# Optimization experiments

Measured on AMD Instinct MI355X. Metric: run time of the kernel, lower is better.

## Reference

```python
import jax, jax.numpy as jnp
import numpy as np

ATTN_SCALE = 0.12
HEAD_DIM = 128


def _rms_norm(x):
    # F.rms_norm with no weight; eps defaults to machine eps of dtype
    eps = jnp.asarray(jnp.finfo(x.dtype).eps, x.dtype)
    return x * jax.lax.rsqrt(jnp.mean(x * x, axis=-1, keepdims=True) + eps)


def _rope(x):
    # x: [B, T, H, D]; standard rotary over (first-half, second-half) pairs
    T, D = x.shape[1], x.shape[-1]
    half = D // 2
    inv_freq = 1.0 / (10000.0 ** (jnp.arange(half, dtype=jnp.float32) / half))
    ang = jnp.arange(T, dtype=jnp.float32)[:, None] * inv_freq[None, :]  # [T, half]
    cos = jnp.cos(ang)[None, :, None, :].astype(x.dtype)
    sin = jnp.sin(ang)[None, :, None, :].astype(x.dtype)
    x1, x2 = x[..., :half], x[..., half:]
    return jnp.concatenate([x1 * cos - x2 * sin, x1 * sin + x2 * cos], axis=-1)


def setup_inputs() -> dict:
    key = jax.random.key(0)
    ks = jax.random.split(key, 4)
    B, T, dim, H, hd = 4, 2048, 1024, 8, HEAD_DIM
    hdim = H * hd
    std = 0.5 * dim ** (-0.5)
    bound = (3.0 ** 0.5) * std
    return {
        "x": jax.random.normal(ks[0], (B, T, dim), jnp.float32),
        "ve": jax.random.normal(ks[1], (B, T, hdim), jnp.float32),
        "qkv_w": jax.random.uniform(ks[2], (3, hdim, dim), jnp.float32, -bound, bound),
        "lambdas": jnp.array([0.5, 0.5], jnp.float32),
        "c_proj_w": jax.random.normal(ks[3], (dim, hdim), jnp.float32) * (hdim ** -0.5),
        "c_proj_b": jnp.zeros((dim,), jnp.float32),
    }


def reference(x, ve, qkv_w, lambdas, c_proj_w, c_proj_b):
    B, T, dim = x.shape
    hdim = qkv_w.shape[1]
    hd = HEAD_DIM
    H = hdim // hd
    # fused QKV projection: [B,T,3,H,hd]
    qkv = jnp.einsum('btd,ehd->bteh', x, qkv_w.reshape(3 * hdim, dim).reshape(3 * H, hd, dim).reshape(3 * hdim // hd, hd, dim))
    qkv = jnp.einsum('btd,fd->btf', x, qkv_w.reshape(3 * hdim, dim)).reshape(B, T, 3, H, hd)
    q, k, v = qkv[:, :, 0], qkv[:, :, 1], qkv[:, :, 2]  # each [B,T,H,hd]
    q, k = _rms_norm(q), _rms_norm(k)
    q, k = _rope(q), _rope(k)
    v = lambdas[0] * v + lambdas[1] * ve.reshape(B, T, H, hd)
    # causal SDPA with custom scale
    scores = jnp.einsum('bthd,bshd->bhts', q, k) * ATTN_SCALE  # [B,H,T,T]
    causal = jnp.tril(jnp.ones((T, T), dtype=bool))
    scores = jnp.where(causal[None, None], scores, jnp.finfo(scores.dtype).min)
    p = jax.nn.softmax(scores, axis=-1)
    y = jnp.einsum('bhts,bshd->bthd', p, v).reshape(B, T, hdim)
    return y @ c_proj_w.T + c_proj_b
```

## Files before the change

kernel.cpp:

```cpp
#include <hip/hip_runtime.h>
#include <math.h>

typedef unsigned short u16;
typedef short bf16x8 __attribute__((ext_vector_type(8)));
typedef u16 u16x2 __attribute__((ext_vector_type(2)));
typedef u16 u16x4 __attribute__((ext_vector_type(4)));
typedef u16 u16x8 __attribute__((ext_vector_type(8)));
typedef float f32x2 __attribute__((ext_vector_type(2)));
typedef float f32x4 __attribute__((ext_vector_type(4)));
typedef float f32x16 __attribute__((ext_vector_type(16)));

typedef __attribute__((address_space(1))) const void gvoid_t;
typedef __attribute__((address_space(3))) void lvoid_t;

__device__ __forceinline__ u16 f2bf(float f) {
  union { float f; unsigned u; } v; v.f = f;
  unsigned r = v.u + 0x7fffu + ((v.u >> 16) & 1u);
  return (u16)(r >> 16);
}
__device__ __forceinline__ float bf2f(u16 h) {
  union { unsigned u; float f; } v; v.u = ((unsigned)h) << 16;
  return v.f;
}
__device__ __forceinline__ f32x4 mfma16(bf16x8 a, bf16x8 b, f32x4 c) {
  return __builtin_amdgcn_mfma_f32_16x16x32_bf16(a, b, c, 0, 0, 0);
}
__device__ __forceinline__ f32x16 mfma32(bf16x8 a, bf16x8 b, f32x16 c) {
  return __builtin_amdgcn_mfma_f32_32x32x16_bf16(a, b, c, 0, 0, 0);
}
__device__ __forceinline__ void gload_lds16(const void* g, void* l) {
  __builtin_amdgcn_global_load_lds((gvoid_t*)g, (lvoid_t*)l, 16, 0, 0);
}
__device__ __forceinline__ unsigned cvtpk_bf16(float lo, float hi) {
  unsigned r;
  asm("v_cvt_pk_bf16_f32 %0, %1, %2" : "=v"(r) : "v"(lo), "v"(hi));
  return r;
}
__device__ __forceinline__ void pswap32(unsigned& a, unsigned& b) {
  asm("v_permlane32_swap_b32 %0, %1" : "+v"(a), "+v"(b));
}

#define BAR() __builtin_amdgcn_s_barrier()
#define WAITLGKM()                          \
  asm volatile("s_waitcnt lgkmcnt(0)");     \
  __builtin_amdgcn_sched_barrier(0)
#define WAITVM(N)                                \
  asm volatile("s_waitcnt vmcnt(" #N ")");       \
  __builtin_amdgcn_sched_barrier(0)

__global__ __launch_bounds__(256) void cvt_bf16_kernel(const float* __restrict__ in,
                                                       u16* __restrict__ out, int n4) {
  int i = blockIdx.x * 256 + threadIdx.x;
  if (i >= n4) return;
  f32x4 v = *(const f32x4*)(in + (size_t)i * 4);
  u16x4 o;
  o[0] = f2bf(v[0]); o[1] = f2bf(v[1]); o[2] = f2bf(v[2]); o[3] = f2bf(v[3]);
  *(u16x4*)(out + (size_t)i * 4) = o;
}

__global__ __launch_bounds__(256) void rope_tab_kernel(float* __restrict__ ct,
                                                       float* __restrict__ st) {
  int i = blockIdx.x * 256 + threadIdx.x;
  int t = i >> 6, j = i & 63;
  float inv = powf(10000.f, -(float)j * (1.0f / 64.0f));
  float ang = (float)t * inv;
  ct[i] = cosf(ang);
  st[i] = sinf(ang);
}

template <int BM, int OUTF32>
__global__ __launch_bounds__(512, 1) void gemm8p_kernel(
    const u16* __restrict__ A, const u16* __restrict__ B, void* __restrict__ C,
    const float* __restrict__ bias, int M, int N, int K, int nbn) {
  constexpr int AH = BM / 2;
  constexpr int WR = AH / 2;
  constexpr int MI = WR / 16;
  constexpr int NACC = 2 * MI;
  constexpr int AROUNDS = AH / 64;
  __shared__ u16 Alds[2][BM * 64];
  __shared__ u16 Blds[2][256 * 64];
  int nwg = gridDim.x;
  int cpx = nwg >> 3;
  int bid = blockIdx.x;
  int swz = (bid & 7) * cpx + (bid >> 3);
  int bm = swz / nbn, bn = swz % nbn;
  size_t m0 = (size_t)bm * BM, n0 = (size_t)bn * 256;
  int tid = threadIdx.x, wid = tid >> 6, lane = tid & 63;
  int wr = wid >> 2, wc = wid & 3, l15 = lane & 15, l4 = lane >> 4;
  int srow = tid >> 3, sch = tid & 7;

  const u16* Abase = A + m0 * K;
  const u16* Bbase = B + n0 * K;

  f32x4 acc[NACC][4];
#pragma unroll
  for (int m = 0; m < NACC; m++)
#pragma unroll
    for (int n = 0; n < 4; n++) acc[m][n] = f32x4{0.f, 0.f, 0.f, 0.f};

  auto stageA = [&](int buf, int kt, int half) {
#pragma unroll
    for (int r = 0; r < AROUNDS; ++r) {
      int row = AH * half + 64 * r + srow;
      gload_lds16(Abase + (size_t)row * K + kt * 64 + 8 * (sch ^ (row & 7)),
                  &Alds[buf][(AH * half + 64 * r + 8 * wid) * 64]);
    }
  };
  auto stageB = [&](int buf, int kt, int half) {
#pragma unroll
    for (int r = 0; r < 2; ++r) {
      int row = 128 * half + 64 * r + srow;
      gload_lds16(Bbase + (size_t)row * K + kt * 64 + 8 * (sch ^ (row & 7)),
                  &Blds[buf][(128 * half + 64 * r + 8 * wid) * 64]);
    }
  };
  auto rdA = [&](int buf, int half, bf16x8 (&a)[MI][2]) {
#pragma unroll
    for (int mi = 0; mi < MI; ++mi)
#pragma unroll
      for (int kk = 0; kk < 2; ++kk) {
        int row = AH * half + WR * wr + 16 * mi + l15;
        a[mi][kk] = *(const bf16x8*)((const char*)(&Alds[buf][0]) + row * 128 +
                                     ((kk * 64 + 16 * l4) ^ ((row & 7) << 4)));
      }
  };
  auto rdB = [&](int buf, int half, bf16x8 (&bb)[2][2]) {
#pragma unroll
    for (int ni = 0; ni < 2; ++ni)
#pragma unroll
      for (int kk = 0; kk < 2; ++kk) {
        int row = 64 * wc + 32 * half + 16 * ni + l15;
        bb[ni][kk] = *(const bf16x8*)((const char*)(&Blds[buf][0]) + row * 128 +
                                      ((kk * 64 + 16 * l4) ^ ((row & 7) << 4)));
      }
  };

#define QUAD(AF, BF, MH, NH)                                              \
  do {                                                                    \
    __builtin_amdgcn_s_setprio(1);                                        \
    _Pragma("unroll") for (int mi = 0; mi < MI; ++mi)                     \
        _Pragma("unroll") for (int ni = 0; ni < 2; ++ni)                  \
            _Pragma("unroll") for (int kk = 0; kk < 2; ++kk)              \
                acc[MI * MH + mi][2 * NH + ni] =                          \
        mfma16(AF[mi][kk], BF[ni][kk], acc[MI * MH + mi][2 * NH + ni]);   \
    __builtin_amdgcn_s_setprio(0);                                        \
  } while (0)

  stageB(0, 0, 0);
  stageB(0, 0, 1);
  stageA(0, 0, 0);
  stageA(0, 0, 1);
  if constexpr (BM == 256) { WAITVM(2); } else { WAITVM(1); }
  BAR();

  int nk = K >> 6;
  bf16x8 a0[MI][2], a1[MI][2], b0[2][2], b1[2][2];
  for (int t = 0; t < nk; ++t) {
    int buf = t & 1, nxt = buf ^ 1;
    bool pf = (t + 1 < nk);
    rdA(buf, 0, a0);
    rdB(buf, 0, b0);
    if (pf) stageB(nxt, t + 1, 0);
    BAR();
    WAITLGKM();
    QUAD(a0, b0, 0, 0);
    BAR();
    rdB(buf, 1, b1);
    if (pf) stageB(nxt, t + 1, 1);
    BAR();
    WAITLGKM();
    QUAD(a0, b1, 0, 1);
    if (pf) { WAITVM(4); } else { WAITVM(0); }
    BAR();
    rdA(buf, 1, a1);
    if (pf) stageA(nxt, t + 1, 0);
    BAR();
    WAITLGKM();
    QUAD(a1, b0, 1, 0);
    BAR();
    if (pf) stageA(nxt, t + 1, 1);
    BAR();
    QUAD(a1, b1, 1, 1);
    if (pf) {
      if constexpr (BM == 256) { WAITVM(2); } else { WAITVM(1); }
    }
    BAR();
  }

#pragma unroll
  for (int mi = 0; mi < NACC; ++mi) {
#pragma unroll
    for (int ni = 0; ni < 4; ++ni) {
      size_t row = m0 + AH * (mi / MI) + WR * wr + 16 * (mi % MI) + 4 * l4;
      size_t col = n0 + 64 * wc + 16 * ni + l15;
#pragma unroll
      for (int i = 0; i < 4; ++i) {
        float v = acc[mi][ni][i];
        if constexpr (OUTF32) {
          ((float*)C)[(row + i) * N + col] = v + bias[col];
        } else {
          ((u16*)C)[(row + i) * N + col] = f2bf(v);
        }
      }
    }
  }
#undef QUAD
}

__global__ __launch_bounds__(256) void transform_kernel(
    const u16* __restrict__ qkv, const float* __restrict__ ve,
    const float* __restrict__ lam, const float* __restrict__ ct,
    const float* __restrict__ st, u16* __restrict__ qn, u16* __restrict__ kn,
    u16* __restrict__ vt) {
  constexpr int T = 2048, HD = 128;
  __shared__ u16 vtile[64][132];
  int tt = blockIdx.x, bh = blockIdx.y;
  int b = bh >> 3, h = bh & 7;
  int tid = threadIdx.x, wid = tid >> 6, lane = tid & 63;
  float l0 = lam[0], l1 = lam[1];
  int d0 = 2 * lane;
  float sgn = (lane < 32) ? -1.f : 1.f;
#pragma unroll 1
  for (int j = 0; j < 16; ++j) {
    int tl = wid * 16 + j;
    int t = tt * 64 + tl;
    size_t base = ((size_t)(b * T + t)) * 3072 + h * HD + d0;
    u16x2 qraw = *(const u16x2*)(qkv + base);
    u16x2 kraw = *(const u16x2*)(qkv + base + 1024);
    u16x2 vraw = *(const u16x2*)(qkv + base + 2048);
    f32x2 vef = *(const f32x2*)(ve + ((size_t)(b * T + t)) * 1024 + h * HD + d0);
    float q0 = bf2f(qraw[0]), q1 = bf2f(qraw[1]);
    float k0 = bf2f(kraw[0]), k1 = bf2f(kraw[1]);
    float sq = q0 * q0 + q1 * q1, sk = k0 * k0 + k1 * k1;
#pragma unroll
    for (int m = 1; m < 64; m <<= 1) {
      sq += __shfl_xor(sq, m);
      sk += __shfl_xor(sk, m);
    }
    float qs = rsqrtf(sq * (1.f / 128.f) + 1.1920929e-7f);
    float ks = rsqrtf(sk * (1.f / 128.f) + 1.1920929e-7f);
    q0 *= qs; q1 *= qs; k0 *= ks; k1 *= ks;
    int jj = d0 & 63;
    f32x2 c2 = *(const f32x2*)(ct + t * 64 + jj);
    f32x2 s2 = *(const f32x2*)(st + t * 64 + jj);
    float q0p = __shfl_xor(q0, 32), q1p = __shfl_xor(q1, 32);
    float k0p = __shfl_xor(k0, 32), k1p = __shfl_xor(k1, 32);
    u16x2 oq, ok;
    oq[0] = f2bf(q0 * c2[0] + sgn * q0p * s2[0]);
    oq[1] = f2bf(q1 * c2[1] + sgn * q1p * s2[1]);
    ok[0] = f2bf(k0 * c2[0] + sgn * k0p * s2[0]);
    ok[1] = f2bf(k1 * c2[1] + sgn * k1p * s2[1]);
    size_t orow = ((size_t)bh * T + t) * HD + d0;
    *(u16x2*)(qn + orow) = oq;
    *(u16x2*)(kn + orow) = ok;
    vtile[tl][d0] = f2bf(l0 * bf2f(vraw[0]) + l1 * vef[0]);
    vtile[tl][d0 + 1] = f2bf(l0 * bf2f(vraw[1]) + l1 * vef[1]);
  }
  __syncthreads();
#pragma unroll
  for (int it = 0; it < 4; ++it) {
    int ci = it * 256 + tid;
    int d = ci >> 3, c8 = ci & 7;
    u16x8 o;
#pragma unroll
    for (int u = 0; u < 8; u++) o[u] = vtile[c8 * 8 + u][d];
    *(u16x8*)(vt + ((size_t)bh * HD + d) * T + tt * 64 + c8 * 8) = o;
  }
}

__global__ __launch_bounds__(256, 2) void attn_kernel(
    const u16* __restrict__ Qn, const u16* __restrict__ Kn,
    const u16* __restrict__ Vt, u16* __restrict__ Y) {
  constexpr int T = 2048;
  __shared__ u16 Klds[2][64 * 128];
  __shared__ u16 Vlds[2][128 * 64];
  int bid = blockIdx.x;
  int g = bid >> 5;
  int s = (g < 8) ? (15 - g) : (g - 8);
  int bh = bid & 31;
  int b = bh >> 3, h = bh & 7;
  int tid = threadIdx.x, wid = tid >> 6, lane = tid & 63;
  int l31 = lane & 31, hh = lane >> 5;
  const u16* Qb = Qn + (size_t)bh * T * 128;
  const u16* Kb = Kn + (size_t)bh * T * 128;
  const u16* Vb = Vt + (size_t)bh * 128 * T;
  int q0w = s * 128 + wid * 32;
  int qmaxw = q0w + 31;
  int ktend = 2 * s + 2;
  int qg = q0w + l31;

  bf16x8 qf[8];
  {
    const u16* qr = Qb + (size_t)(q0w + l31) * 128 + 8 * hh;
#pragma unroll
    for (int ks = 0; ks < 8; ks++) qf[ks] = *(const bf16x8*)(qr + 16 * ks);
  }
  f32x16 acc[4];
#pragma unroll
  for (int mt = 0; mt < 4; mt++)
#pragma unroll
    for (int r = 0; r < 16; r++) acc[mt][r] = 0.f;
  float m_run = -1e30f, l_run = 0.f;

  auto stage = [&](int buf, int kt) {
#pragma unroll
    for (int it = 0; it < 4; ++it) {
      int id = wid * 256 + it * 64 + lane;
      int r = id >> 4, c = id & 15;
      gload_lds16(Kb + (size_t)(kt * 64 + r) * 128 + 8 * (c ^ (r & 7)),
                  &Klds[buf][(size_t)(wid * 256 + it * 64) * 8]);
      int rv = id >> 3, cv = id & 7;
      gload_lds16(Vb + (size_t)rv * T + kt * 64 + 8 * (cv ^ (rv & 7)),
                  &Vlds[buf][(size_t)(wid * 256 + it * 64) * 8]);
    }
  };

  stage(0, 0);
  __syncthreads();

  for (int kt = 0; kt < ktend; ++kt) {
    int cur = kt & 1;
    if (kt + 1 < ktend) stage(cur ^ 1, kt + 1);
    if (kt * 64 <= qmaxw) {
      const char* kb = (const char*)&Klds[cur][0];
      const char* vb = (const char*)&Vlds[cur][0];
      int rswz = (l31 & 7) << 4;
      f32x16 st0, st1;
#pragma unroll
      for (int r = 0; r < 16; r++) { st0[r] = 0.f; st1[r] = 0.f; }
#pragma unroll
      for (int ks = 0; ks < 8; ks++) {
        bf16x8 kf0 = *(const bf16x8*)(kb + ((l31 * 256 + 32 * ks + 16 * hh) ^ rswz));
        bf16x8 kf1 = *(const bf16x8*)(kb + (((32 + l31) * 256 + 32 * ks + 16 * hh) ^ rswz));
        st0 = mfma32(kf0, qf[ks], st0);
        st1 = mfma32(kf1, qf[ks], st1);
      }
      bool edge = (kt == (qmaxw >> 6));
      if (edge) {
#pragma unroll
        for (int r = 0; r < 16; r++) {
          int kvb = kt * 64 + (r & 3) + 8 * (r >> 2) + 4 * hh;
          if (kvb > qg) st0[r] = -1e30f;
          if (kvb + 32 > qg) st1[r] = -1e30f;
        }
      }
      float m8[8];
#pragma unroll
      for (int r = 0; r < 8; r++)
        m8[r] = fmaxf(fmaxf(st0[r], st0[r + 8]), fmaxf(st1[r], st1[r + 8]));
#pragma unroll
      for (int r = 0; r < 4; r++) m8[r] = fmaxf(m8[r], m8[r + 4]);
      float pm = fmaxf(fmaxf(m8[0], m8[1]), fmaxf(m8[2], m8[3]));
      pm = fmaxf(pm, __shfl_xor(pm, 32));
      float pmn = pm * 0.12f;
      bool nos = __all(pmn <= m_run + 8.0f);
      float mnew = nos ? m_run : fmaxf(m_run, pmn);
      if (!nos) {
        float alpha = __expf(m_run - mnew);
        l_run *= alpha;
#pragma unroll
        for (int mt = 0; mt < 4; mt++)
#pragma unroll
          for (int r = 0; r < 16; r++) acc[mt][r] *= alpha;
        m_run = mnew;
      }
      float sa = 0.f, sb = 0.f, sc = 0.f, sd = 0.f;
#pragma unroll
      for (int r = 0; r < 4; r++) {
        st0[r]      = __expf(fmaf(st0[r],      0.12f, -mnew)); sa += st0[r];
        st0[r + 4]  = __expf(fmaf(st0[r + 4],  0.12f, -mnew)); sb += st0[r + 4];
        st0[r + 8]  = __expf(fmaf(st0[r + 8],  0.12f, -mnew)); sc += st0[r + 8];
        st0[r + 12] = __expf(fmaf(st0[r + 12], 0.12f, -mnew)); sd += st0[r + 12];
        st1[r]      = __expf(fmaf(st1[r],      0.12f, -mnew)); sa += st1[r];
        st1[r + 4]  = __expf(fmaf(st1[r + 4],  0.12f, -mnew)); sb += st1[r + 4];
        st1[r + 8]  = __expf(fmaf(st1[r + 8],  0.12f, -mnew)); sc += st1[r + 8];
        st1[r + 12] = __expf(fmaf(st1[r + 12], 0.12f, -mnew)); sd += st1[r + 12];
      }
      float ps = (sa + sb) + (sc + sd);
      ps += __shfl_xor(ps, 32);
      l_run += ps;
      unsigned pA0[4], pB0[4], pA1[4], pB1[4];
#pragma unroll
      for (int rr = 0; rr < 4; rr++) {
        pA0[rr] = cvtpk_bf16(st0[4 * rr], st0[4 * rr + 1]);
        pB0[rr] = cvtpk_bf16(st0[4 * rr + 2], st0[4 * rr + 3]);
        pA1[rr] = cvtpk_bf16(st1[4 * rr], st1[4 * rr + 1]);
        pB1[rr] = cvtpk_bf16(st1[4 * rr + 2], st1[4 * rr + 3]);
      }
      bf16x8 pf[4];
#pragma unroll
      for (int ks2 = 0; ks2 < 4; ks2++) {
        int k1 = ks2 & 1;
        unsigned a0, b0, a1, b1;
        if (ks2 < 2) { a0 = pA0[2 * k1]; b0 = pA0[2 * k1 + 1]; a1 = pB0[2 * k1]; b1 = pB0[2 * k1 + 1]; }
        else         { a0 = pA1[2 * k1]; b0 = pA1[2 * k1 + 1]; a1 = pB1[2 * k1]; b1 = pB1[2 * k1 + 1]; }
        pswap32(a0, b0);
        pswap32(a1, b1);
        union { unsigned w[4]; bf16x8 v; } u;
        u.w[0] = a0; u.w[1] = a1; u.w[2] = b0; u.w[3] = b1;
        pf[ks2] = u.v;
      }
#pragma unroll
      for (int mt = 0; mt < 4; mt++) {
        int row = 32 * mt + l31;
#pragma unroll
        for (int ks2 = 0; ks2 < 4; ks2++) {
          bf16x8 vf = *(const bf16x8*)(vb + ((row * 128 + 32 * ks2 + 16 * hh) ^ rswz));
          acc[mt] = mfma32(vf, pf[ks2], acc[mt]);
        }
      }
    }
    __syncthreads();
  }
  float linv = 1.f / l_run;
  size_t yrow = (size_t)b * T + q0w + l31;
  u16* yp = Y + yrow * 1024 + h * 128;
#pragma unroll
  for (int mt = 0; mt < 4; mt++) {
#pragma unroll
    for (int rr = 0; rr < 4; rr++) {
      u16x4 o;
#pragma unroll
      for (int i = 0; i < 4; i++) o[i] = f2bf(acc[mt][4 * rr + i] * linv);
      *(u16x4*)(yp + 32 * mt + 8 * rr + 4 * hh) = o;
    }
  }
}

extern "C" void kernel_launch(void* const* d_in, const int* in_sizes, int n_in,
                              void* d_out, int out_size, void* d_ws, size_t ws_size,
                              hipStream_t stream) {
  (void)in_sizes; (void)n_in; (void)out_size; (void)ws_size;
  const float* x = (const float*)d_in[0];
  const float* ve = (const float*)d_in[1];
  const float* qkvw = (const float*)d_in[2];
  const float* lam = (const float*)d_in[3];
  const float* cpw = (const float*)d_in[4];
  const float* cpb = (const float*)d_in[5];
  float* out = (float*)d_out;
  char* ws = (char*)d_ws;

  u16* xb   = (u16*)(ws + 0);
  u16* wqkv = (u16*)(ws + 16777216);
  u16* wp   = (u16*)(ws + 23068672);
  u16* qkv  = (u16*)(ws + 25165824);
  u16* qn   = (u16*)(ws + 75497472);
  u16* kn   = (u16*)(ws + 92274688);
  u16* vt   = (u16*)(ws + 109051904);
  float* ctab = (float*)(ws + 125829120);
  float* stab = (float*)(ws + 126353408);
  u16* y = xb;

  rope_tab_kernel<<<512, 256, 0, stream>>>(ctab, stab);
  cvt_bf16_kernel<<<8192, 256, 0, stream>>>(x, xb, 2097152);
  cvt_bf16_kernel<<<3072, 256, 0, stream>>>(qkvw, wqkv, 786432);
  cvt_bf16_kernel<<<1024, 256, 0, stream>>>(cpw, wp, 262144);
  gemm8p_kernel<128, 0><<<768, 512, 0, stream>>>(xb, wqkv, qkv, nullptr, 8192, 3072, 1024, 12);
  transform_kernel<<<dim3(32, 32), 256, 0, stream>>>(qkv, ve, lam, ctab, stab, qn, kn, vt);
  attn_kernel<<<512, 256, 0, stream>>>(qn, kn, vt, y);
  gemm8p_kernel<128, 1><<<256, 512, 0, stream>>>(y, wp, out, cpb, 8192, 1024, 1024, 4);
}
```

Measured before the change: 209.8 us.

## Rework GEMM prefetch schedule, vectorize transform, use exp2 softmax and MFMA priority

The GEMM now issues the A and B prefetches for the next K-tile earlier and interleaved, with vmcnt waits computed from per-stage load counts. The QKV GEMM switches to BM=256 tiles with half the workgroups. The transform kernel is vectorized to 8 elements per lane using 16-lane row groups, with a padded LDS tile. The attention softmax uses hardware exp2 with a pre-scaled log2e factor, and the MFMA blocks are raised in wave priority. Together these target global-load latency, instruction count and scheduling, at the risk of wrong vmcnt accounting and changed occupancy or tile balance.

```diff
diff --git a/kernel.cpp b/kernel.cpp
--- a/kernel.cpp
+++ b/kernel.cpp
@@ -40,13 +40,25 @@
   asm("v_permlane32_swap_b32 %0, %1" : "+v"(a), "+v"(b));
 }
 
+#if __has_builtin(__builtin_amdgcn_exp2f)
+#define EXPW(x) __builtin_amdgcn_exp2f(x)
+#define SCALE_W 0.17312354f
+#define DEFER_THR 11.5415603f
+#else
+#define EXPW(x) __expf(x)
+#define SCALE_W 0.12f
+#define DEFER_THR 8.0f
+#endif
+
 #define BAR() __builtin_amdgcn_s_barrier()
 #define WAITLGKM()                          \
   asm volatile("s_waitcnt lgkmcnt(0)");     \
   __builtin_amdgcn_sched_barrier(0)
-#define WAITVM(N)                                \
-  asm volatile("s_waitcnt vmcnt(" #N ")");       \
-  __builtin_amdgcn_sched_barrier(0)
+#define WAITVMC(N)                                    \
+  do {                                                \
+    __builtin_amdgcn_s_waitcnt(0x0F70 | (N));         \
+    __builtin_amdgcn_sched_barrier(0);                \
+  } while (0)
 
 __global__ __launch_bounds__(256) void cvt_bf16_kernel(const float* __restrict__ in,
                                                        u16* __restrict__ out, int n4) {
@@ -77,6 +89,8 @@
   constexpr int MI = WR / 16;
   constexpr int NACC = 2 * MI;
   constexpr int AROUNDS = AH / 64;
+  constexpr int SA = AROUNDS;
+  constexpr int SB = 2;
   __shared__ u16 Alds[2][BM * 64];
   __shared__ u16 Blds[2][256 * 64];
   int nwg = gridDim.x;
@@ -147,10 +161,10 @@
   } while (0)
 
   stageB(0, 0, 0);
+  stageA(0, 0, 0);
   stageB(0, 0, 1);
-  stageA(0, 0, 0);
   stageA(0, 0, 1);
-  if constexpr (BM == 256) { WAITVM(2); } else { WAITVM(1); }
+  WAITVMC(SA + SB);
   BAR();
 
   int nk = K >> 6;
@@ -160,30 +174,27 @@
     bool pf = (t + 1 < nk);
     rdA(buf, 0, a0);
     rdB(buf, 0, b0);
-    if (pf) stageB(nxt, t + 1, 0);
+    if (pf) { stageB(nxt, t + 1, 0); stageA(nxt, t + 1, 0); }
     BAR();
     WAITLGKM();
     QUAD(a0, b0, 0, 0);
+    if (pf) { WAITVMC(2 * SA + SB); } else { WAITVMC(SA); }
     BAR();
     rdB(buf, 1, b1);
     if (pf) stageB(nxt, t + 1, 1);
     BAR();
     WAITLGKM();
     QUAD(a0, b1, 0, 1);
-    if (pf) { WAITVM(4); } else { WAITVM(0); }
+    if (pf) { WAITVMC(2 * SB + SA); } else { WAITVMC(0); }
     BAR();
     rdA(buf, 1, a1);
-    if (pf) stageA(nxt, t + 1, 0);
+    if (pf) stageA(nxt, t + 1, 1);
     BAR();
     WAITLGKM();
     QUAD(a1, b0, 1, 0);
     BAR();
-    if (pf) stageA(nxt, t + 1, 1);
-    BAR();
     QUAD(a1, b1, 1, 1);
-    if (pf) {
-      if constexpr (BM == 256) { WAITVM(2); } else { WAITVM(1); }
-    }
+    if (pf) WAITVMC(SA + SB);
     BAR();
   }
 
@@ -212,49 +223,62 @@
     const float* __restrict__ lam, const float* __restrict__ ct,
     const float* __restrict__ st, u16* __restrict__ qn, u16* __restrict__ kn,
     u16* __restrict__ vt) {
-  constexpr int T = 2048, HD = 128;
-  __shared__ u16 vtile[64][132];
+  constexpr int T = 2048;
+  __shared__ u16 vtile[64][136];
   int tt = blockIdx.x, bh = blockIdx.y;
   int b = bh >> 3, h = bh & 7;
   int tid = threadIdx.x, wid = tid >> 6, lane = tid & 63;
+  int lsub = lane & 15, lrow = lane >> 4;
   float l0 = lam[0], l1 = lam[1];
-  int d0 = 2 * lane;
-  float sgn = (lane < 32) ? -1.f : 1.f;
-#pragma unroll 1
-  for (int j = 0; j < 16; ++j) {
-    int tl = wid * 16 + j;
+  int d0 = 8 * lsub;
+  float sgn = (lsub < 8) ? -1.f : 1.f;
+  int jj = d0 & 63;
+#pragma unroll
+  for (int it = 0; it < 4; ++it) {
+    int tl = wid * 16 + it * 4 + lrow;
     int t = tt * 64 + tl;
-    size_t base = ((size_t)(b * T + t)) * 3072 + h * HD + d0;
-    u16x2 qraw = *(const u16x2*)(qkv + base);
-    u16x2 kraw = *(const u16x2*)(qkv + base + 1024);
-    u16x2 vraw = *(const u16x2*)(qkv + base + 2048);
-    f32x2 vef = *(const f32x2*)(ve + ((size_t)(b * T + t)) * 1024 + h * HD + d0);
-    float q0 = bf2f(qraw[0]), q1 = bf2f(qraw[1]);
-    float k0 = bf2f(kraw[0]), k1 = bf2f(kraw[1]);
-    float sq = q0 * q0 + q1 * q1, sk = k0 * k0 + k1 * k1;
-#pragma unroll
-    for (int m = 1; m < 64; m <<= 1) {
+    size_t base = ((size_t)(b * T + t)) * 3072 + h * 128 + d0;
+    u16x8 qraw = *(const u16x8*)(qkv + base);
+    u16x8 kraw = *(const u16x8*)(qkv + base + 1024);
+    u16x8 vraw = *(const u16x8*)(qkv + base + 2048);
+    const float* vep = ve + ((size_t)(b * T + t)) * 1024 + h * 128 + d0;
+    f32x4 ve0 = *(const f32x4*)(vep);
+    f32x4 ve1 = *(const f32x4*)(vep + 4);
+    float q[8], k[8];
+    float sq = 0.f, sk = 0.f;
+#pragma unroll
+    for (int i = 0; i < 8; ++i) {
+      q[i] = bf2f(qraw[i]); k[i] = bf2f(kraw[i]);
+      sq += q[i] * q[i]; sk += k[i] * k[i];
+    }
+#pragma unroll
+    for (int m = 1; m < 16; m <<= 1) {
       sq += __shfl_xor(sq, m);
       sk += __shfl_xor(sk, m);
     }
     float qs = rsqrtf(sq * (1.f / 128.f) + 1.1920929e-7f);
     float ks = rsqrtf(sk * (1.f / 128.f) + 1.1920929e-7f);
-    q0 *= qs; q1 *= qs; k0 *= ks; k1 *= ks;
-    int jj = d0 & 63;
-    f32x2 c2 = *(const f32x2*)(ct + t * 64 + jj);
-    f32x2 s2 = *(const f32x2*)(st + t * 64 + jj);
-    float q0p = __shfl_xor(q0, 32), q1p = __shfl_xor(q1, 32);
-    float k0p = __shfl_xor(k0, 32), k1p = __shfl_xor(k1, 32);
-    u16x2 oq, ok;
-    oq[0] = f2bf(q0 * c2[0] + sgn * q0p * s2[0]);
-    oq[1] = f2bf(q1 * c2[1] + sgn * q1p * s2[1]);
-    ok[0] = f2bf(k0 * c2[0] + sgn * k0p * s2[0]);
-    ok[1] = f2bf(k1 * c2[1] + sgn * k1p * s2[1]);
-    size_t orow = ((size_t)bh * T + t) * HD + d0;
-    *(u16x2*)(qn + orow) = oq;
-    *(u16x2*)(kn + orow) = ok;
-    vtile[tl][d0] = f2bf(l0 * bf2f(vraw[0]) + l1 * vef[0]);
-    vtile[tl][d0 + 1] = f2bf(l0 * bf2f(vraw[1]) + l1 * vef[1]);
+#pragma unroll
+    for (int i = 0; i < 8; ++i) { q[i] *= qs; k[i] *= ks; }
+    f32x4 c0 = *(const f32x4*)(ct + t * 64 + jj);
+    f32x4 c1 = *(const f32x4*)(ct + t * 64 + jj + 4);
+    f32x4 s0 = *(const f32x4*)(st + t * 64 + jj);
+    f32x4 s1 = *(const f32x4*)(st + t * 64 + jj + 4);
+    u16x8 oq, ok, ov;
+#pragma unroll
+    for (int i = 0; i < 8; ++i) {
+      float qp = __shfl_xor(q[i], 8), kp = __shfl_xor(k[i], 8);
+      float cc = (i < 4) ? c0[i & 3] : c1[i & 3];
+      float ss = (i < 4) ? s0[i & 3] : s1[i & 3];
+      oq[i] = f2bf(q[i] * cc + sgn * qp * ss);
+      ok[i] = f2bf(k[i] * cc + sgn * kp * ss);
+      float vv = (i < 4) ? ve0[i & 3] : ve1[i & 3];
+      ov[i] = f2bf(l0 * bf2f(vraw[i]) + l1 * vv);
+    }
+    size_t orow = ((size_t)bh * T + t) * 128 + d0;
+    *(u16x8*)(qn + orow) = oq;
+    *(u16x8*)(kn + orow) = ok;
+    *(u16x8*)&vtile[tl][d0] = ov;
   }
   __syncthreads();
 #pragma unroll
@@ -264,7 +288,7 @@
     u16x8 o;
 #pragma unroll
     for (int u = 0; u < 8; u++) o[u] = vtile[c8 * 8 + u][d];
-    *(u16x8*)(vt + ((size_t)bh * HD + d) * T + tt * 64 + c8 * 8) = o;
+    *(u16x8*)(vt + ((size_t)bh * 128 + d) * T + tt * 64 + c8 * 8) = o;
   }
 }
 
@@ -328,6 +352,7 @@
       f32x16 st0, st1;
 #pragma unroll
       for (int r = 0; r < 16; r++) { st0[r] = 0.f; st1[r] = 0.f; }
+      __builtin_amdgcn_s_setprio(1);
 #pragma unroll
       for (int ks = 0; ks < 8; ks++) {
         bf16x8 kf0 = *(const bf16x8*)(kb + ((l31 * 256 + 32 * ks + 16 * hh) ^ rswz));
@@ -335,6 +360,7 @@
         st0 = mfma32(kf0, qf[ks], st0);
         st1 = mfma32(kf1, qf[ks], st1);
       }
+      __builtin_amdgcn_s_setprio(0);
       bool edge = (kt == (qmaxw >> 6));
       if (edge) {
 #pragma unroll
@@ -352,11 +378,11 @@
       for (int r = 0; r < 4; r++) m8[r] = fmaxf(m8[r], m8[r + 4]);
       float pm = fmaxf(fmaxf(m8[0], m8[1]), fmaxf(m8[2], m8[3]));
       pm = fmaxf(pm, __shfl_xor(pm, 32));
-      float pmn = pm * 0.12f;
-      bool nos = __all(pmn <= m_run + 8.0f);
+      float pmn = pm * SCALE_W;
+      bool nos = __all(pmn <= m_run + DEFER_THR);
       float mnew = nos ? m_run : fmaxf(m_run, pmn);
       if (!nos) {
-        float alpha = __expf(m_run - mnew);
+        float alpha = EXPW(m_run - mnew);
         l_run *= alpha;
 #pragma unroll
         for (int mt = 0; mt < 4; mt++)
@@ -367,14 +393,14 @@
       float sa = 0.f, sb = 0.f, sc = 0.f, sd = 0.f;
 #pragma unroll
       for (int r = 0; r < 4; r++) {
-        st0[r]      = __expf(fmaf(st0[r],      0.12f, -mnew)); sa += st0[r];
-        st0[r + 4]  = __expf(fmaf(st0[r + 4],  0.12f, -mnew)); sb += st0[r + 4];
-        st0[r + 8]  = __expf(fmaf(st0[r + 8],  0.12f, -mnew)); sc += st0[r + 8];
-        st0[r + 12] = __expf(fmaf(st0[r + 12], 0.12f, -mnew)); sd += st0[r + 12];
-        st1[r]      = __expf(fmaf(st1[r],      0.12f, -mnew)); sa += st1[r];
-        st1[r + 4]  = __expf(fmaf(st1[r + 4],  0.12f, -mnew)); sb += st1[r + 4];
-        st1[r + 8]  = __expf(fmaf(st1[r + 8],  0.12f, -mnew)); sc += st1[r + 8];
-        st1[r + 12] = __expf(fmaf(st1[r + 12], 0.12f, -mnew)); sd += st1[r + 12];
+        st0[r]      = EXPW(fmaf(st0[r],      SCALE_W, -mnew)); sa += st0[r];
+        st0[r + 4]  = EXPW(fmaf(st0[r + 4],  SCALE_W, -mnew)); sb += st0[r + 4];
+        st0[r + 8]  = EXPW(fmaf(st0[r + 8],  SCALE_W, -mnew)); sc += st0[r + 8];
+        st0[r + 12] = EXPW(fmaf(st0[r + 12], SCALE_W, -mnew)); sd += st0[r + 12];
+        st1[r]      = EXPW(fmaf(st1[r],      SCALE_W, -mnew)); sa += st1[r];
+        st1[r + 4]  = EXPW(fmaf(st1[r + 4],  SCALE_W, -mnew)); sb += st1[r + 4];
+        st1[r + 8]  = EXPW(fmaf(st1[r + 8],  SCALE_W, -mnew)); sc += st1[r + 8];
+        st1[r + 12] = EXPW(fmaf(st1[r + 12], SCALE_W, -mnew)); sd += st1[r + 12];
       }
       float ps = (sa + sb) + (sc + sd);
       ps += __shfl_xor(ps, 32);
@@ -400,6 +426,7 @@
         u.w[0] = a0; u.w[1] = a1; u.w[2] = b0; u.w[3] = b1;
         pf[ks2] = u.v;
       }
+      __builtin_amdgcn_s_setprio(1);
 #pragma unroll
       for (int mt = 0; mt < 4; mt++) {
         int row = 32 * mt + l31;
@@ -409,6 +436,7 @@
           acc[mt] = mfma32(vf, pf[ks2], acc[mt]);
         }
       }
+      __builtin_amdgcn_s_setprio(0);
     }
     __syncthreads();
   }
@@ -455,7 +483,7 @@
   cvt_bf16_kernel<<<8192, 256, 0, stream>>>(x, xb, 2097152);
   cvt_bf16_kernel<<<3072, 256, 0, stream>>>(qkvw, wqkv, 786432);
   cvt_bf16_kernel<<<1024, 256, 0, stream>>>(cpw, wp, 262144);
-  gemm8p_kernel<128, 0><<<768, 512, 0, stream>>>(xb, wqkv, qkv, nullptr, 8192, 3072, 1024, 12);
+  gemm8p_kernel<256, 0><<<384, 512, 0, stream>>>(xb, wqkv, qkv, nullptr, 8192, 3072, 1024, 12);
   transform_kernel<<<dim3(32, 32), 256, 0, stream>>>(qkv, ve, lam, ctab, stab, qn, kn, vt);
   attn_kernel<<<512, 256, 0, stream>>>(qn, kn, vt, y);
   gemm8p_kernel<128, 1><<<256, 512, 0, stream>>>(y, wp, out, cpb, 8192, 1024, 1024, 4);
```

New measurement: 203.5 us. 3.0% less time.
